# Kernel optimization log

Hardware: AMD Instinct MI355X
Metric: run time of the kernel (lower is better)

The kernel has to match this reference:

```python
import jax, jax.numpy as jnp
import numpy as np

# Fixed problem configuration (regularized ragged structure)
B = 8192      # number of trajectories
D = 32        # input_size
H = 128       # hidden_size
PH = 64       # p_hidden
PREP = 10     # prep_hidden
CS = 8        # cov_size
CH = 32       # cov_hidden
NT = 16       # number of observation times
NO = 4096     # observations per time (trajectories observed)
DT = 0.1      # delta_t (1 euler step between consecutive obs times)
NPOST = 4     # euler steps after last observation up to T
LOGC = float(np.log(np.sqrt(2.0 * np.pi)))


def setup_inputs() -> dict:
    key = jax.random.key(0)
    ks = jax.random.split(key, 24)
    f32 = jnp.float32

    def rn(k, shape, fan_in):
        return jax.random.normal(k, shape, f32) / np.sqrt(fan_in)

    X = jax.random.normal(ks[0], (NT, NO, D), f32)
    M = (jax.random.uniform(ks[1], (NT, NO, D)) < 0.7).astype(f32)  # 0/1 observation mask
    # unique trajectory indices per observation time -> deterministic scatter
    obs_idx = jax.vmap(lambda k: jax.random.permutation(k, B)[:NO])(
        jax.random.split(ks[2], NT)).astype(jnp.int32)
    cov = jax.random.normal(ks[3], (B, CS), f32)

    inp = dict(X=X, M=M, obs_idx=obs_idx, cov=cov)
    # covariates_map: Linear(CS,CH) ReLU Linear(CH,H) Tanh
    inp['cm_w1'] = rn(ks[4], (CS, CH), CS);  inp['cm_b1'] = jnp.zeros((CH,), f32)
    inp['cm_w2'] = rn(ks[5], (CH, H), CH);   inp['cm_b2'] = jnp.zeros((H,), f32)
    # p_model: Linear(H,PH) ReLU Linear(PH,2D)
    inp['p_w1'] = rn(ks[6], (H, PH), H);     inp['p_b1'] = jnp.zeros((PH,), f32)
    inp['p_w2'] = rn(ks[7], (PH, 2 * D), PH); inp['p_b2'] = jnp.zeros((2 * D,), f32)
    # GRUODECell with input 2D
    inp['xz_w'] = rn(ks[8], (2 * D, H), 2 * D); inp['xz_b'] = jnp.zeros((H,), f32)
    inp['hz_w'] = rn(ks[9], (H, H), H)
    inp['xn_w'] = rn(ks[10], (2 * D, H), 2 * D); inp['xn_b'] = jnp.zeros((H,), f32)
    inp['hn_w'] = rn(ks[11], (H, H), H)
    # GRUCell(PREP*D, H): stored as [in, 3H] / [H, 3H], chunk order r,z,n
    inp['w_ih'] = rn(ks[12], (PREP * D, 3 * H), PREP * D)
    inp['w_hh'] = rn(ks[13], (H, 3 * H), H)
    inp['b_ih'] = jnp.zeros((3 * H,), f32)
    inp['b_hh'] = jnp.zeros((3 * H,), f32)
    # observation preprocessing
    std = np.sqrt(2.0 / (4 + PREP))
    inp['w_prep'] = std * jax.random.normal(ks[14], (D, 4, PREP), f32)
    inp['bias_prep'] = 0.1 + jnp.zeros((D, PREP), f32)
    return inp


def reference(X, M, obs_idx, cov,
              cm_w1, cm_b1, cm_w2, cm_b2,
              p_w1, p_b1, p_w2, p_b2,
              xz_w, xz_b, hz_w, xn_w, xn_b, hn_w,
              w_ih, w_hh, b_ih, b_hh, w_prep, bias_prep):
    def p_model(h):
        return jax.nn.relu(h @ p_w1 + p_b1) @ p_w2 + p_b2

    def gru_ode(p, h):  # returns dh/dt as in GRUODECell
        z = jax.nn.sigmoid(p @ xz_w + xz_b + h @ hz_w)
        n = jnp.tanh(p @ xn_w + xn_b + (z * h) @ hn_w)
        return (1.0 - z) * (n - h)

    def gru_cell(x, h):  # torch nn.GRUCell semantics, chunks r,z,n
        gi = x @ w_ih + b_ih
        gh = h @ w_hh + b_hh
        ir, iz, inn = jnp.split(gi, 3, axis=1)
        hr, hz, hn = jnp.split(gh, 3, axis=1)
        r = jax.nn.sigmoid(ir + hr)
        z = jax.nn.sigmoid(iz + hz)
        n = jnp.tanh(inn + r * hn)
        return (1.0 - z) * n + z * h

    h = jnp.tanh(jax.nn.relu(cov @ cm_w1 + cm_b1) @ cm_w2 + cm_b2)  # [B,H]
    p = p_model(h)                                                   # [B,2D]
    loss = jnp.float32(0.0)

    for t in range(NT):
        # one euler ODE step up to the observation time
        h = h + DT * gru_ode(p, h)
        p = p_model(h)
        # Bayesian jump at observed trajectories
        idx = obs_idx[t]            # [NO]
        Xo, Mo = X[t], M[t]         # [NO,D]
        po = p[idx]                 # gather [NO,2D]
        mean, logvar = jnp.split(po, 2, axis=1)
        sigma = jnp.exp(0.5 * logvar)
        err = (Xo - mean) / sigma
        loss = loss + (0.5 * ((err ** 2 + logvar + 2.0 * LOGC) * Mo)).sum()
        feats = jnp.stack([Xo, mean, logvar, err], axis=-1)          # [NO,D,4]
        gin = jax.nn.relu(jnp.einsum('ndf,dfp->ndp', feats, w_prep) + bias_prep)
        gin = (gin * Mo[:, :, None]).reshape(NO, D * PREP)
        h = h.at[idx].set(gru_cell(gin, h[idx]))                     # scatter update
        p = p_model(h)

    for _ in range(NPOST):  # evolve to horizon T
        h = h + DT * gru_ode(p, h)
        p = p_model(h)

    return h, p, loss
```

## Files before the change

### kernel.cpp

```cpp
#include <hip/hip_runtime.h>

#define B_     8192
#define D_     32
#define H_     128
#define PH_    64
#define PREP_  10
#define CS_    8
#define CH_    32
#define NT_    16
#define NO_    4096
#define NPOST_ 4
#define DT_    0.1f
#define TWO_LOGC 1.8378770664093453f

#define OFF_XZXN 0
#define OFF_HZ   16384
#define OFF_HN   32768
#define OFF_PW1  49152
#define OFF_PW2  57344
#define OFF_WIH  61440
#define OFF_WHH  184320
#define BLOB_ELEMS 233472
#define INV_BYTE_OFF ((size_t)BLOB_ELEMS*2)
#define WJP_BYTE_OFF (INV_BYTE_OFF + 262144)

#define WL_XZXN 0
#define WL_HZ   16384
#define WL_PW1  32768
#define WL_PW2  40960
#define WL_TOT  45056

#define STRH 136
#define STRP 72
#define STRG 328
#define PFSTR 67

#define SB_XZ    0
#define SB_XN    128
#define SB_P1    256
#define SB_P2    320
#define SB_BRZ   384
#define SB_BIN   640
#define SB_BHN   768
#define SB_TOT   896

typedef float f4  __attribute__((ext_vector_type(4)));
typedef short bf8 __attribute__((ext_vector_type(8)));

__device__ __forceinline__ f4 mfma16(bf8 a, bf8 b, f4 c){
  return __builtin_amdgcn_mfma_f32_16x16x32_bf16(a,b,c,0,0,0);
}
__device__ __forceinline__ unsigned short f2bf(float f){
  unsigned int u = __builtin_bit_cast(unsigned int, f);
  u = (u + 0x7FFFu + ((u>>16)&1u)) >> 16;
  return (unsigned short)u;
}
__device__ __forceinline__ unsigned int cvtpk(float lo, float hi){
  unsigned int r;
  asm("v_cvt_pk_bf16_f32 %0, %1, %2" : "=v"(r) : "v"(lo), "v"(hi));
  return r;
}
__device__ __forceinline__ float sigmoidf_(float x){ return 1.f/(1.f+__expf(-x)); }
__device__ __forceinline__ float tanhf_(float x){
  float e = __expf(2.f*x);
  return 1.f - 2.f/(e+1.f);
}
__device__ __forceinline__ int permk(int k){
  return ((k>>5)<<5) | (((k>>2)&3)<<3) | (((k>>4)&1)<<2) | (k&3);
}

template<int NKC,int NSEL,int NTT,int NRT>
__device__ __forceinline__ void gemmW(f4 (&acc)[NRT][NSEL], const unsigned short* Ald,
                                      int strideUsh, const unsigned short* __restrict__ Bg,
                                      int lane, int tile0){
  const int lc = lane & 15, a4 = lane >> 4;
  const unsigned short* a0 = Ald + lc*strideUsh + a4*8;
  const unsigned short* bl = Bg + (size_t)tile0*512 + lane*8;
  #pragma unroll 2
  for(int kc=0;kc<NKC;kc++){
    bf8 av0 = *(const bf8*)(a0 + kc*32);
    bf8 av1;
    if constexpr(NRT==2) av1 = *(const bf8*)(a0 + 16*strideUsh + kc*32);
    #pragma unroll
    for(int s=0;s<NSEL;s++){
      bf8 bv = *(const bf8*)(bl + (size_t)(kc*NTT + s*8)*512);
      acc[0][s] = mfma16(av0, bv, acc[0][s]);
      if constexpr(NRT==2) acc[1][s] = mfma16(av1, bv, acc[1][s]);
    }
  }
}

__global__ void init_inv(unsigned short* inv, float* outLoss){
  int i = blockIdx.x*256 + threadIdx.x;
  if(i < NT_*B_) inv[i] = 0xFFFFu;
  if(i == 0) *outLoss = 0.f;
}

__global__ void scatter_inv(unsigned short* inv, const int* __restrict__ obs){
  int i = blockIdx.x*256 + threadIdx.x;
  if(i < NT_*NO_){
    int t = i >> 12;
    int o = i & 4095;
    inv[(size_t)t*B_ + obs[i]] = (unsigned short)o;
  }
}

__global__ void build_blobs(const float* __restrict__ pw1, const float* __restrict__ pw2,
                            const float* __restrict__ xzw, const float* __restrict__ xnw,
                            const float* __restrict__ hzw, const float* __restrict__ hnw,
                            const float* __restrict__ wih, const float* __restrict__ whh,
                            const float* __restrict__ wprep, const float* __restrict__ bprep,
                            const float* __restrict__ pb2, const float* __restrict__ xzb,
                            const float* __restrict__ xnb,
                            unsigned short* __restrict__ blob, float* __restrict__ wjp){
  int sec = blockIdx.y;
  int e = blockIdx.x*256 + threadIdx.x;
  if(sec==7){
    if(e < 32*51){
      int d = e/51, r = e%51, pr = r/5, c = r%5;
      float v = 0.f;
      if(pr < PREP_) v = (c<4) ? wprep[d*40 + c*10 + pr] : bprep[d*10 + pr];
      wjp[e] = v;
    } else if(e < 32*51 + 256){
      int n = e - 32*51;
      float acc = (n<128)? xzb[n] : xnb[n-128];
      for(int m=0;m<2*D_;m++){
        float xz = (n<128)? xzw[(size_t)m*H_+n] : xnw[(size_t)m*H_+(n-128)];
        acc += pb2[m]*xz;
      }
      wjp[e] = acc;
    }
    return;
  }
  const float* src=nullptr; int N, ld, off, cnt;
  switch(sec){
    case 0: src=nullptr; N=256; ld=0;   off=OFF_XZXN; cnt=16384;  break;
    case 1: src=hzw;  N=128; ld=128; off=OFF_HZ;   cnt=16384;  break;
    case 2: src=hnw;  N=128; ld=128; off=OFF_HN;   cnt=16384;  break;
    case 3: src=pw1;  N=64;  ld=64;  off=OFF_PW1;  cnt=8192;   break;
    case 4: src=pw2;  N=64;  ld=64;  off=OFF_PW2;  cnt=4096;   break;
    case 5: src=wih;  N=384; ld=384; off=OFF_WIH;  cnt=122880; break;
    default:src=whh;  N=384; ld=384; off=OFF_WHH;  cnt=49152;  break;
  }
  if(e >= cnt) return;
  int ntiles = N >> 4;
  int perkc = ntiles << 9;
  int kc = e / perkc, rem = e % perkc;
  int nt = rem >> 9, li = rem & 511;
  int lane = li >> 3, j = li & 7;
  int n = nt*16 + (lane & 15);
  int k = kc*32 + ((lane>>4)&3)*4 + (j&3) + ((j>>2)<<4);
  float v;
  if(sec==0){
    float acc = 0.f;
    #pragma unroll 4
    for(int m=0;m<2*D_;m++){
      float xz = (n<128)? xzw[(size_t)m*H_+n] : xnw[(size_t)m*H_+(n-128)];
      acc += pw2[(size_t)k*(2*D_)+m]*xz;
    }
    v = acc;
  }
  else v = src[(size_t)k*ld + n];
  blob[off + e] = f2bf(v);
}

__global__ __launch_bounds__(512,2) void fused(
    const float* __restrict__ X, const float* __restrict__ M,
    const float* __restrict__ cov,
    const float* __restrict__ cm_w1, const float* __restrict__ cm_b1,
    const float* __restrict__ cm_w2, const float* __restrict__ cm_b2,
    const float* __restrict__ p_b1, const float* __restrict__ p_b2,
    const float* __restrict__ b_ih, const float* __restrict__ b_hh,
    const unsigned short* __restrict__ blob, const float* __restrict__ wjp,
    const unsigned short* __restrict__ inv,
    float* __restrict__ outH, float* __restrict__ outP, float* __restrict__ outLoss)
{
  __shared__ __align__(16) unsigned short wlds[WL_TOT];
  __shared__ __align__(16) unsigned short hb[32*STRH];
  __shared__ __align__(16) unsigned short qb[32*STRP];
  __shared__ __align__(16) unsigned short un[32*STRG];
  __shared__ __align__(16) float pf32[32*PFSTR];
  __shared__ float sb[SB_TOT];
  __shared__ float sbJ[32*51];
  __shared__ int obsO[32];
  __shared__ float lred[8];

  const int tid  = threadIdx.x;
  const int lane = tid & 63;
  const int w    = tid >> 6;
  const int lc   = lane & 15;
  const int a4   = lane >> 4;
  const int base = blockIdx.x * 32;
  float lsum = 0.f;

  const float* fb = wjp + 32*51;
  for(int i=tid;i<128;i+=512){ sb[SB_XZ+i]=fb[i]; sb[SB_XN+i]=fb[128+i];
                               sb[SB_BIN+i]=b_ih[256+i]; sb[SB_BHN+i]=b_hh[256+i]; }
  for(int i=tid;i<64;i+=512){ sb[SB_P1+i]=p_b1[i]; sb[SB_P2+i]=p_b2[i]; }
  for(int i=tid;i<256;i+=512) sb[SB_BRZ+i]=b_ih[i]+b_hh[i];
  for(int i=tid;i<32*51;i+=512) sbJ[i]=wjp[i];
  for(int i=tid*8;i<32768;i+=4096) *(uint4*)(wlds+i)      = *(const uint4*)(blob+i);
  for(int i=tid*8;i<12288;i+=4096) *(uint4*)(wlds+32768+i)= *(const uint4*)(blob+49152+i);

  {
    float* c1f = pf32;
    float* hInitF = (float*)un;
    int row = tid>>4, q = tid&15;
    float a[2];
    #pragma unroll
    for(int j=0;j<2;j++) a[j]=cm_b1[q*2+j];
    #pragma unroll
    for(int k=0;k<CS_;k++){
      float cv = cov[(size_t)(base+row)*CS_+k];
      #pragma unroll
      for(int j=0;j<2;j++) a[j] += cv*cm_w1[k*CH_+q*2+j];
    }
    #pragma unroll
    for(int j=0;j<2;j++) c1f[row*36+q*2+j] = fmaxf(a[j],0.f);
    __syncthreads();
    float acc2[8];
    #pragma unroll
    for(int j=0;j<8;j++) acc2[j]=cm_b2[q*8+j];
    for(int k=0;k<CH_;k++){
      float cv = c1f[row*36+k];
      #pragma unroll
      for(int j=0;j<8;j++) acc2[j] += cv*cm_w2[k*H_+q*8+j];
    }
    #pragma unroll
    for(int j=0;j<8;j++) hInitF[row*132+q*8+j] = tanhf_(acc2[j]);
    __syncthreads();
  }

  f4 hFr[2];
  f4 pFr;
  const int prt = w & 1, pct = w >> 1;
  {
    float* hInitF = (float*)un;
    #pragma unroll
    for(int rt=0;rt<2;rt++)
      #pragma unroll
      for(int g=0;g<4;g++)
        hFr[rt][g] = hInitF[(rt*16+a4*4+g)*132 + w*16+lc];
    __syncthreads();
    #pragma unroll
    for(int rt=0;rt<2;rt++)
      #pragma unroll
      for(int g=0;g<4;g++)
        hb[(rt*16+a4*4+g)*STRH + permk(w*16+lc)] = f2bf(hFr[rt][g]);
    __syncthreads();
  }

  auto qphase = [&](){
    f4 acc[1][1];
    { float bv = sb[SB_P1 + pct*16+lc]; f4 t={bv,bv,bv,bv}; acc[0][0]=t; }
    gemmW<4,1,4,1>(acc, hb + prt*16*STRH, STRH, wlds+WL_PW1, lane, pct);
    #pragma unroll
    for(int g=0;g<4;g++)
      qb[(prt*16+a4*4+g)*STRP + permk(pct*16+lc)] = f2bf(fmaxf(acc[0][0][g],0.f));
    __syncthreads();
  };

  auto pphase = [&](bool fin){
    f4 acc[1][1];
    { float bv = sb[SB_P2 + pct*16+lc]; f4 t={bv,bv,bv,bv}; acc[0][0]=t; }
    gemmW<2,1,4,1>(acc, qb + prt*16*STRP, STRP, wlds+WL_PW2, lane, pct);
    if(fin) pFr = acc[0][0];
    #pragma unroll
    for(int g=0;g<4;g++)
      pf32[(prt*16+a4*4+g)*PFSTR + pct*16+lc] = acc[0][0][g];
    __syncthreads();
  };

  auto euler = [&](){
    bf8 hnB[4];
    #pragma unroll
    for(int kc=0;kc<4;kc++)
      hnB[kc] = *(const bf8*)(blob + OFF_HN + (size_t)(kc*8+w)*512 + lane*8);
    f4 ax[2][2];
    #pragma unroll
    for(int rt=0;rt<2;rt++){
      float bz = sb[SB_XZ + w*16+lc], bn = sb[SB_XN + w*16+lc];
      f4 tz={bz,bz,bz,bz}, tn={bn,bn,bn,bn};
      ax[rt][0]=tz; ax[rt][1]=tn;
    }
    gemmW<2,2,16,2>(ax, qb, STRP, wlds+WL_XZXN, lane, w);
    f4 ah[2][1]; { f4 z4={0.f,0.f,0.f,0.f}; ah[0][0]=z4; ah[1][0]=z4; }
    gemmW<4,1,8,2>(ah, hb, STRH, wlds+WL_HZ, lane, w);
    f4 zr[2];
    #pragma unroll
    for(int rt=0;rt<2;rt++)
      #pragma unroll
      for(int g=0;g<4;g++){
        float z = sigmoidf_(ax[rt][0][g] + ah[rt][0][g]);
        zr[rt][g]=z;
        un[(rt*16+a4*4+g)*STRH + permk(w*16+lc)] = f2bf(z*hFr[rt][g]);
      }
    __syncthreads();
    f4 ah2[2]; { f4 z4={0.f,0.f,0.f,0.f}; ah2[0]=z4; ah2[1]=z4; }
    {
      const unsigned short* a0 = un + lc*STRH + a4*8;
      #pragma unroll
      for(int kc=0;kc<4;kc++){
        bf8 av0 = *(const bf8*)(a0 + kc*32);
        bf8 av1 = *(const bf8*)(a0 + 16*STRH + kc*32);
        ah2[0] = mfma16(av0, hnB[kc], ah2[0]);
        ah2[1] = mfma16(av1, hnB[kc], ah2[1]);
      }
    }
    #pragma unroll
    for(int rt=0;rt<2;rt++)
      #pragma unroll
      for(int g=0;g<4;g++){
        float nn = tanhf_(ax[rt][1][g] + ah2[rt][g]);
        float ho = hFr[rt][g];
        float hv = ho + DT_*(1.f-zr[rt][g])*(nn-ho);
        hFr[rt][g]=hv;
        hb[(rt*16+a4*4+g)*STRH + permk(w*16+lc)] = f2bf(hv);
      }
    __syncthreads();
  };

  auto jump = [&](int o0, int o1, float x0, float m0, float x1, float m1){
    bf8 pre[3];
    #pragma unroll
    for(int s=0;s<3;s++)
      pre[s] = *(const bf8*)(blob + OFF_WIH + (size_t)(w + s*8)*512 + lane*8);
    f4 gh[2][3];
    #pragma unroll
    for(int rt=0;rt<2;rt++){
      float bhn = sb[SB_BHN + w*16+lc];
      f4 z4={0.f,0.f,0.f,0.f}, tn={bhn,bhn,bhn,bhn};
      gh[rt][0]=z4; gh[rt][1]=z4; gh[rt][2]=tn;
    }
    gemmW<4,3,24,2>(gh, hb, STRH, blob+OFF_WHH, lane, w);
    {
      int rp = tid>>5, d = tid&31;
      int row0 = rp*2, row1 = rp*2+1;
      if(d==0){ obsO[row0]=o0; obsO[row1]=o1; }
      float mean0 = pf32[row0*PFSTR + d], lv0 = pf32[row0*PFSTR + D_ + d];
      float mean1 = pf32[row1*PFSTR + d], lv1 = pf32[row1*PFSTR + D_ + d];
      float er0 = (x0-mean0)*__expf(-0.5f*lv0);
      float er1 = (x1-mean1)*__expf(-0.5f*lv1);
      lsum += 0.5f*((er0*er0 + lv0 + TWO_LOGC)*m0 + (er1*er1 + lv1 + TWO_LOGC)*m1);
      const float* wj = sbJ + d*51;
      unsigned short* g0 = un + row0*STRG;
      unsigned short* g1 = un + row1*STRG;
      #pragma unroll
      for(int pr=0;pr<PREP_;pr+=2){
        const float* ca = wj + pr*5;
        const float* cb = ca + 5;
        float sa0 = fmaxf(x0*ca[0] + mean0*ca[1] + lv0*ca[2] + er0*ca[3] + ca[4], 0.f)*m0;
        float sb0 = fmaxf(x0*cb[0] + mean0*cb[1] + lv0*cb[2] + er0*cb[3] + cb[4], 0.f)*m0;
        float sa1 = fmaxf(x1*ca[0] + mean1*ca[1] + lv1*ca[2] + er1*ca[3] + ca[4], 0.f)*m1;
        float sb1 = fmaxf(x1*cb[0] + mean1*cb[1] + lv1*cb[2] + er1*cb[3] + cb[4], 0.f)*m1;
        int pos = permk(d*PREP_ + pr);
        *(unsigned int*)(g0 + pos) = cvtpk(sa0, sb0);
        *(unsigned int*)(g1 + pos) = cvtpk(sa1, sb1);
      }
    }
    __syncthreads();
    f4 gi[2][3];
    #pragma unroll
    for(int rt=0;rt<2;rt++){
      float br = sb[SB_BRZ + w*16+lc], bz = sb[SB_BRZ+128 + w*16+lc], bn = sb[SB_BIN + w*16+lc];
      f4 tr={br,br,br,br}, tz={bz,bz,bz,bz}, tn={bn,bn,bn,bn};
      gi[rt][0]=tr; gi[rt][1]=tz; gi[rt][2]=tn;
    }
    {
      const unsigned short* A = un + lc*STRG + a4*8;
      bf8 av0 = *(const bf8*)(A);
      bf8 av1 = *(const bf8*)(A + 16*STRG);
      #pragma unroll
      for(int s=0;s<3;s++){
        gi[0][s] = mfma16(av0, pre[s], gi[0][s]);
        gi[1][s] = mfma16(av1, pre[s], gi[1][s]);
      }
    }
    gemmW<9,3,24,2>(gi, un+32, STRG, blob+OFF_WIH + 24*512, lane, w);
    #pragma unroll
    for(int rt=0;rt<2;rt++)
      #pragma unroll
      for(int g=0;g<4;g++){
        int row = rt*16+a4*4+g;
        float r = sigmoidf_(gi[rt][0][g] + gh[rt][0][g]);
        float z = sigmoidf_(gi[rt][1][g] + gh[rt][1][g]);
        float nn = tanhf_(gi[rt][2][g] + r*gh[rt][2][g]);
        float hv = (1.f-z)*nn + z*hFr[rt][g];
        if(obsO[row]>=0){
          hFr[rt][g]=hv;
          hb[row*STRH + permk(w*16+lc)] = f2bf(hv);
        }
      }
    __syncthreads();
  };

  qphase();
  for(int t=0;t<NT_;t++){
    int rp = tid>>5, d = tid&31;
    unsigned short iv0 = inv[(size_t)t*B_ + base + rp*2];
    unsigned short iv1 = inv[(size_t)t*B_ + base + rp*2 + 1];
    int o0 = (iv0==0xFFFFu)? -1 : (int)iv0;
    int o1 = (iv1==0xFFFFu)? -1 : (int)iv1;
    float x0=0.f,m0=0.f,x1=0.f,m1=0.f;
    if(o0>=0){
      x0 = X[((size_t)t*NO_+o0)*D_ + d];
      m0 = M[((size_t)t*NO_+o0)*D_ + d];
    }
    if(o1>=0){
      x1 = X[((size_t)t*NO_+o1)*D_ + d];
      m1 = M[((size_t)t*NO_+o1)*D_ + d];
    }
    euler();
    qphase();
    pphase(false);
    jump(o0, o1, x0, m0, x1, m1);
    qphase();
  }
  for(int it=0;it<NPOST_;it++){
    euler();
    qphase();
  }
  pphase(true);

  #pragma unroll
  for(int rt=0;rt<2;rt++)
    #pragma unroll
    for(int g=0;g<4;g++)
      outH[(size_t)(base + rt*16+a4*4+g)*H_ + w*16+lc] = hFr[rt][g];
  #pragma unroll
  for(int g=0;g<4;g++)
    outP[(size_t)(base + prt*16+a4*4+g)*(2*D_) + pct*16+lc] = pFr[g];

  #pragma unroll
  for(int off=32;off>0;off>>=1) lsum += __shfl_down(lsum, off);
  if(lane==0) lred[w]=lsum;
  __syncthreads();
  if(tid==0){
    float s = 0.f;
    #pragma unroll
    for(int i=0;i<8;i++) s += lred[i];
    atomicAdd(outLoss, s);
  }
}

extern "C" void kernel_launch(void* const* d_in, const int* in_sizes, int n_in,
                              void* d_out, int out_size, void* d_ws, size_t ws_size,
                              hipStream_t stream){
  const float* X      = (const float*)d_in[0];
  const float* M      = (const float*)d_in[1];
  const int*   obs    = (const int*)  d_in[2];
  const float* cov    = (const float*)d_in[3];
  const float* cm_w1  = (const float*)d_in[4];
  const float* cm_b1  = (const float*)d_in[5];
  const float* cm_w2  = (const float*)d_in[6];
  const float* cm_b2  = (const float*)d_in[7];
  const float* p_w1   = (const float*)d_in[8];
  const float* p_b1   = (const float*)d_in[9];
  const float* p_w2   = (const float*)d_in[10];
  const float* p_b2   = (const float*)d_in[11];
  const float* xz_w   = (const float*)d_in[12];
  const float* xz_b   = (const float*)d_in[13];
  const float* hz_w   = (const float*)d_in[14];
  const float* xn_w   = (const float*)d_in[15];
  const float* xn_b   = (const float*)d_in[16];
  const float* hn_w   = (const float*)d_in[17];
  const float* w_ih   = (const float*)d_in[18];
  const float* w_hh   = (const float*)d_in[19];
  const float* b_ih   = (const float*)d_in[20];
  const float* b_hh   = (const float*)d_in[21];
  const float* w_prep = (const float*)d_in[22];
  const float* bprep  = (const float*)d_in[23];

  unsigned short* blob = (unsigned short*)d_ws;
  unsigned short* inv  = (unsigned short*)((char*)d_ws + INV_BYTE_OFF);
  float*          wjp  = (float*)((char*)d_ws + WJP_BYTE_OFF);
  float* outH = (float*)d_out;
  float* outP = outH + (size_t)B_*H_;
  float* outLoss = outP + (size_t)B_*2*D_;

  init_inv   <<<dim3((NT_*B_+255)/256), dim3(256), 0, stream>>>(inv, outLoss);
  scatter_inv<<<dim3((NT_*NO_+255)/256), dim3(256), 0, stream>>>(inv, obs);
  build_blobs<<<dim3(480,8), dim3(256), 0, stream>>>(p_w1,p_w2,xz_w,xn_w,hz_w,hn_w,w_ih,w_hh,
                                                     w_prep,bprep,p_b2,xz_b,xn_b, blob, wjp);
  fused      <<<dim3(B_/32), dim3(512), 0, stream>>>(
      X, M, cov, cm_w1, cm_b1, cm_w2, cm_b2, p_b1, p_b2,
      b_ih, b_hh, blob, wjp, inv, outH, outP, outLoss);
}
```

Before: 176.8 us.

## Fuse p-model second layer into jump phase with per-warp redundant compute

Removes the separate pphase and its block-wide barrier inside the time loop. Each warp now computes the full 64-wide second p_model layer for its 16-row tile and writes only its own 4 rows into a private LDS slab, which the jump phase then reads without a __syncthreads. This costs redundant MFMA work (4 output tiles per warp instead of 1) in exchange for one fewer barrier and better overlap with the W_hh GEMM.

```diff
diff --git a/kernel.cpp b/kernel.cpp
--- a/kernel.cpp
+++ b/kernel.cpp
@@ -33,7 +33,6 @@
 #define STRH 136
 #define STRP 72
 #define STRG 328
-#define PFSTR 67
 
 #define SB_XZ    0
 #define SB_XN    128
@@ -69,7 +68,7 @@
   return ((k>>5)<<5) | (((k>>2)&3)<<3) | (((k>>4)&1)<<2) | (k&3);
 }
 
-template<int NKC,int NSEL,int NTT,int NRT>
+template<int NKC,int NSEL,int NTT,int NRT,int TSTR=8>
 __device__ __forceinline__ void gemmW(f4 (&acc)[NRT][NSEL], const unsigned short* Ald,
                                       int strideUsh, const unsigned short* __restrict__ Bg,
                                       int lane, int tile0){
@@ -83,7 +82,7 @@
     if constexpr(NRT==2) av1 = *(const bf8*)(a0 + 16*strideUsh + kc*32);
     #pragma unroll
     for(int s=0;s<NSEL;s++){
-      bf8 bv = *(const bf8*)(bl + (size_t)(kc*NTT + s*8)*512);
+      bf8 bv = *(const bf8*)(bl + (size_t)(kc*NTT + s*TSTR)*512);
       acc[0][s] = mfma16(av0, bv, acc[0][s]);
       if constexpr(NRT==2) acc[1][s] = mfma16(av1, bv, acc[1][s]);
     }
@@ -179,7 +178,7 @@
   __shared__ __align__(16) unsigned short hb[32*STRH];
   __shared__ __align__(16) unsigned short qb[32*STRP];
   __shared__ __align__(16) unsigned short un[32*STRG];
-  __shared__ __align__(16) float pf32[32*PFSTR];
+  __shared__ __align__(16) float wp[8*272];
   __shared__ float sb[SB_TOT];
   __shared__ float sbJ[32*51];
   __shared__ int obsO[32];
@@ -203,7 +202,7 @@
   for(int i=tid*8;i<12288;i+=4096) *(uint4*)(wlds+32768+i)= *(const uint4*)(blob+49152+i);
 
   {
-    float* c1f = pf32;
+    float* c1f = wp;
     float* hInitF = (float*)un;
     int row = tid>>4, q = tid&15;
     float a[2];
@@ -257,17 +256,6 @@
     #pragma unroll
     for(int g=0;g<4;g++)
       qb[(prt*16+a4*4+g)*STRP + permk(pct*16+lc)] = f2bf(fmaxf(acc[0][0][g],0.f));
-    __syncthreads();
-  };
-
-  auto pphase = [&](bool fin){
-    f4 acc[1][1];
-    { float bv = sb[SB_P2 + pct*16+lc]; f4 t={bv,bv,bv,bv}; acc[0][0]=t; }
-    gemmW<2,1,4,1>(acc, qb + prt*16*STRP, STRP, wlds+WL_PW2, lane, pct);
-    if(fin) pFr = acc[0][0];
-    #pragma unroll
-    for(int g=0;g<4;g++)
-      pf32[(prt*16+a4*4+g)*PFSTR + pct*16+lc] = acc[0][0][g];
     __syncthreads();
   };
 
@@ -334,11 +322,26 @@
     }
     gemmW<4,3,24,2>(gh, hb, STRH, blob+OFF_WHH, lane, w);
     {
-      int rp = tid>>5, d = tid&31;
-      int row0 = rp*2, row1 = rp*2+1;
+      f4 pa[1][4];
+      #pragma unroll
+      for(int s=0;s<4;s++){ float bv = sb[SB_P2 + s*16+lc]; f4 t={bv,bv,bv,bv}; pa[0][s]=t; }
+      gemmW<2,4,4,1,1>(pa, qb + (w>>2)*16*STRP, STRP, wlds+WL_PW2, lane, 0);
+      if(a4 == (w&3)){
+        float* wpW = wp + w*272;
+        #pragma unroll
+        for(int s=0;s<4;s++)
+          #pragma unroll
+          for(int g=0;g<4;g++)
+            wpW[g*68 + s*16 + lc] = pa[0][s][g];
+      }
+    }
+    {
+      const float* wpW = wp + w*272;
+      int rl0 = 2*(lane>>5), d = lane&31;
+      int row0 = 4*w + rl0, row1 = row0 + 1;
       if(d==0){ obsO[row0]=o0; obsO[row1]=o1; }
-      float mean0 = pf32[row0*PFSTR + d], lv0 = pf32[row0*PFSTR + D_ + d];
-      float mean1 = pf32[row1*PFSTR + d], lv1 = pf32[row1*PFSTR + D_ + d];
+      float mean0 = wpW[rl0*68 + d],     lv0 = wpW[rl0*68 + 32 + d];
+      float mean1 = wpW[(rl0+1)*68 + d], lv1 = wpW[(rl0+1)*68 + 32 + d];
       float er0 = (x0-mean0)*__expf(-0.5f*lv0);
       float er1 = (x1-mean1)*__expf(-0.5f*lv1);
       lsum += 0.5f*((er0*er0 + lv0 + TWO_LOGC)*m0 + (er1*er1 + lv1 + TWO_LOGC)*m1);
@@ -412,7 +415,6 @@
     }
     euler();
     qphase();
-    pphase(false);
     jump(o0, o1, x0, m0, x1, m1);
     qphase();
   }
@@ -420,7 +422,12 @@
     euler();
     qphase();
   }
-  pphase(true);
+  {
+    f4 acc[1][1];
+    { float bv = sb[SB_P2 + pct*16+lc]; f4 t={bv,bv,bv,bv}; acc[0][0]=t; }
+    gemmW<2,1,4,1>(acc, qb + prt*16*STRP, STRP, wlds+WL_PW2, lane, pct);
+    pFr = acc[0][0];
+  }
 
   #pragma unroll
   for(int rt=0;rt<2;rt++)
```

Result: slower. 182.1 us, median of 2 (+3.0%).
